# Performance work log

Measured on AMD Instinct MI355X. Metric: run time of the kernel, lower is better.

## Reference

```python
import jax, jax.numpy as jnp
import numpy as np

B, S, HID = 1, 2048, 2048
H, D = 16, 128
CACHE = 2048


def _rotate_half(x):
    x1, x2 = jnp.split(x, 2, axis=-1)
    return jnp.concatenate([-x2, x1], axis=-1)


def setup_inputs() -> dict:
    key = jax.random.key(0)
    ks = jax.random.split(key, 10)
    sc = 1.0 / np.sqrt(HID)
    return {
        "x": jax.random.normal(ks[0], (B, S, HID), jnp.float32),
        "wq": jax.random.normal(ks[1], (HID, H * D), jnp.float32) * sc,
        "wk": jax.random.normal(ks[2], (HID, H * D), jnp.float32) * sc,
        "wv": jax.random.normal(ks[3], (HID, H * D), jnp.float32) * sc,
        "wo": jax.random.normal(ks[4], (H * D, HID), jnp.float32) * sc,
        "cos": jax.random.uniform(ks[5], (1, 1, S, D), jnp.float32),
        "sin": jax.random.uniform(ks[6], (1, 1, S, D), jnp.float32),
        "attention_mask": jnp.zeros((B, 1, S, CACHE + S), jnp.float32),
        "k_cache": jax.random.normal(ks[7], (B, H, CACHE, D), jnp.float32),
        "v_cache": jax.random.normal(ks[8], (B, H, CACHE, D), jnp.float32),
    }


def reference(x, wq, wk, wv, wo, cos, sin, attention_mask, k_cache, v_cache):
    b, s, _ = x.shape
    # QKV projections -> [B, H, S, D]
    q = (x @ wq).reshape(b, s, H, D).transpose(0, 2, 1, 3)
    k = (x @ wk).reshape(b, s, H, D).transpose(0, 2, 1, 3)
    v = (x @ wv).reshape(b, s, H, D).transpose(0, 2, 1, 3)
    # inline RoPE (rotate-half)
    q = q * cos + _rotate_half(q) * sin
    k = k * cos + _rotate_half(k) * sin
    # KV-cache concat along sequence dim
    k = jnp.concatenate([k_cache, k], axis=2)
    v = jnp.concatenate([v_cache, v], axis=2)
    # manual scaled dot-product attention
    scale = 1.0 / np.sqrt(D).astype(np.float32)
    scores = jnp.einsum("bhqd,bhkd->bhqk", q, k) * scale + attention_mask
    attn = jax.nn.softmax(scores, axis=-1)
    ctx = jnp.einsum("bhqk,bhkd->bhqd", attn, v)  # [B,H,S,D]
    ctx = ctx.transpose(0, 2, 1, 3).reshape(b, s, H * D)
    return ctx @ wo
```

## Files before the change

### kernel.cpp

```cpp
#include <hip/hip_runtime.h>
#include <hip/hip_bf16.h>
#include <hip/hip_fp16.h>


typedef _Float16 half_t;
typedef __attribute__((ext_vector_type(8))) _Float16 f16x8;
typedef __attribute__((ext_vector_type(4))) _Float16 f16x4;
typedef __attribute__((ext_vector_type(4))) float f32x4;
typedef __attribute__((ext_vector_type(16))) float f32x16;

#define HIDN 2048
#define SEQ  2048
#define NH   16
#define HD   128
#define KVL  4096

#define VMCNT(n) asm volatile("s_waitcnt vmcnt(" #n ")" ::: "memory")

__device__ __forceinline__ void gll16(const void* g, void* l) {
  __builtin_amdgcn_global_load_lds(
      (const __attribute__((address_space(1))) void*)g,
      (__attribute__((address_space(3))) void*)l, 16, 0, 0);
}

__device__ __forceinline__ int pkrtz(float a, float b) {
  auto t = __builtin_amdgcn_cvt_pkrtz(a, b);
  return __builtin_bit_cast(int, t);
}

__global__ void k_prep(const float* __restrict__ x, half_t* __restrict__ x16,
                       const float* __restrict__ wq, const float* __restrict__ wk,
                       const float* __restrict__ wv, const float* __restrict__ wo,
                       half_t* __restrict__ wt_qkv, half_t* __restrict__ wt_o,
                       const float* __restrict__ kc, half_t* __restrict__ Kb,
                       const float* __restrict__ vc, half_t* __restrict__ Vt) {
  __shared__ float tile[64][65];
  int b = blockIdx.x;
  if (b < 2048) {
    int i = (b * 256 + threadIdx.x) * 8;
    float4 a = *reinterpret_cast<const float4*>(x + i);
    float4 c = *reinterpret_cast<const float4*>(x + i + 4);
    f16x8 o;
    o[0]=(half_t)a.x; o[1]=(half_t)a.y; o[2]=(half_t)a.z; o[3]=(half_t)a.w;
    o[4]=(half_t)c.x; o[5]=(half_t)c.y; o[6]=(half_t)c.z; o[7]=(half_t)c.w;
    *reinterpret_cast<f16x8*>(x16 + i) = o;
  } else if (b < 6144) {
    int idx = b - 2048;
    int z = idx >> 10, local = idx & 1023;
    int nx = local & 31, ky = local >> 5;
    const float* src = (z == 0) ? wq : (z == 1) ? wk : (z == 2) ? wv : wo;
    half_t* dst = (z < 3) ? (wt_qkv + (size_t)z * HIDN * HIDN) : wt_o;
    int n0 = nx * 64, k0 = ky * 64;
    int tx = threadIdx.x & 63, ty = threadIdx.x >> 6;
    #pragma unroll
    for (int j = 0; j < 64; j += 4) tile[ty + j][tx] = src[(k0 + ty + j) * HIDN + n0 + tx];
    __syncthreads();
    int ch = threadIdx.x & 7, nl = threadIdx.x >> 3;
    #pragma unroll
    for (int p = 0; p < 2; ++p) {
      int n_ = nl + p * 32;
      f16x8 v;
      #pragma unroll
      for (int e = 0; e < 8; ++e) v[e] = (half_t)tile[ch * 8 + e][n_];
      *reinterpret_cast<f16x8*>(&dst[(n0 + n_) * HIDN + k0 + ch * 8]) = v;
    }
  } else if (b < 8192) {
    int i = ((b - 6144) * 256 + threadIdx.x) * 8;
    int h = i >> 18, rem = i & 262143;
    float4 a = *reinterpret_cast<const float4*>(kc + i);
    float4 c = *reinterpret_cast<const float4*>(kc + i + 4);
    f16x8 o;
    o[0]=(half_t)a.x; o[1]=(half_t)a.y; o[2]=(half_t)a.z; o[3]=(half_t)a.w;
    o[4]=(half_t)c.x; o[5]=(half_t)c.y; o[6]=(half_t)c.z; o[7]=(half_t)c.w;
    *reinterpret_cast<f16x8*>(Kb + h * (KVL * HD) + rem) = o;
  } else {
    int idx = b - 8192;
    int kvx = idx & 31, dy = (idx >> 5) & 1, h = idx >> 6;
    int kv0 = kvx * 64, d0 = dy * 64;
    int tx = threadIdx.x & 63, ty = threadIdx.x >> 6;
    const float* src = vc + h * (2048 * HD);
    #pragma unroll
    for (int j = 0; j < 64; j += 4) tile[ty + j][tx] = src[(kv0 + ty + j) * HD + d0 + tx];
    __syncthreads();
    half_t* dst = Vt + h * (HD * KVL);
    int ch = threadIdx.x & 7, dl = threadIdx.x >> 3;
    #pragma unroll
    for (int p = 0; p < 2; ++p) {
      int d_ = dl + p * 32;
      f16x8 v;
      #pragma unroll
      for (int e = 0; e < 8; ++e) v[e] = (half_t)tile[ch * 8 + e][d_];
      *reinterpret_cast<f16x8*>(&dst[(d0 + d_) * KVL + kv0 + ch * 8]) = v;
    }
  }
}

__global__ void k_rope(half_t* __restrict__ Qb, half_t* __restrict__ Kb,
                       const float* __restrict__ cosb, const float* __restrict__ sinb) {
  int i = blockIdx.x * 256 + threadIdx.x;
  int s = i >> 10;
  int h = (i >> 6) & 15;
  int d = i & 63;
  float c1 = cosb[s * HD + d],      s1 = sinb[s * HD + d];
  float c2 = cosb[s * HD + d + 64], s2 = sinb[s * HD + d + 64];
  half_t* qp = Qb + s * HIDN + h * HD + d;
  float q1 = (float)qp[0], q2 = (float)qp[64];
  qp[0]  = (half_t)(q1 * c1 - q2 * s1);
  qp[64] = (half_t)(q2 * c2 + q1 * s2);
  half_t* kp = Kb + h * (KVL * HD) + (2048 + s) * HD + d;
  float k1 = (float)kp[0], k2 = (float)kp[64];
  kp[0]  = (half_t)(k1 * c1 - k2 * s1);
  kp[64] = (half_t)(k2 * c2 + k1 * s2);
}

__global__ __launch_bounds__(512, 1)
void k_gemm256(const half_t* __restrict__ A, const half_t* __restrict__ B,
               half_t* __restrict__ oQ, half_t* __restrict__ oK, half_t* __restrict__ oV) {
  __shared__ __align__(16) half_t sm[4][2][256 * 32];
  const int Kd = HIDN;
  int bx = blockIdx.x;
  int swz = (bx & 7) * 24 + (bx >> 3);
  int mt = swz / 24, nt = swz % 24;
  int m0 = mt * 256, n0 = nt * 256;
  int tid = threadIdx.x;
  int w = tid >> 6, l = tid & 63, lr = l & 15, lg = l >> 4;
  int waveM = (w >> 2) * 128, waveN = (w & 3) * 64;

  int r0 = tid >> 2, sl = tid & 3;
  const half_t* As0 = A + (m0 + r0) * Kd + ((sl ^ ((r0 >> 1) & 3)) * 8);
  const half_t* As1 = A + (m0 + r0 + 128) * Kd + ((sl ^ ((r0 >> 1) & 3)) * 8);
  const half_t* Bs0 = B + (n0 + r0) * Kd + ((sl ^ ((r0 >> 1) & 3)) * 8);
  const half_t* Bs1 = B + (n0 + r0 + 128) * Kd + ((sl ^ ((r0 >> 1) & 3)) * 8);

  f32x4 acc[8][4] = {};

  auto stage = [&](int buf, int kt) {
    int k0 = kt * 32;
    gll16(As0 + k0, (half_t*)sm[buf][0] + tid * 8);
    gll16(As1 + k0, (half_t*)sm[buf][0] + 4096 + tid * 8);
    gll16(Bs0 + k0, (half_t*)sm[buf][1] + tid * 8);
    gll16(Bs1 + k0, (half_t*)sm[buf][1] + 4096 + tid * 8);
  };
  auto compute = [&](int buf) {
    const half_t* Asm = sm[buf][0];
    const half_t* Bsm = sm[buf][1];
    f16x8 a[8], b2[4];
    #pragma unroll
    for (int f = 0; f < 8; ++f) {
      int rm = waveM + f * 16 + lr;
      a[f] = *reinterpret_cast<const f16x8*>(Asm + rm * 32 + ((lg ^ ((rm >> 1) & 3)) * 8));
    }
    #pragma unroll
    for (int f = 0; f < 4; ++f) {
      int rn = waveN + f * 16 + lr;
      b2[f] = *reinterpret_cast<const f16x8*>(Bsm + rn * 32 + ((lg ^ ((rn >> 1) & 3)) * 8));
    }
    #pragma unroll
    for (int fm = 0; fm < 8; ++fm)
      #pragma unroll
      for (int fn = 0; fn < 4; ++fn)
        acc[fm][fn] = __builtin_amdgcn_mfma_f32_16x16x32_f16(a[fm], b2[fn], acc[fm][fn], 0, 0, 0);
  };

  const int NKt = Kd / 32;
  stage(0, 0);
  stage(1, 1);
  for (int kt = 0; kt < NKt; ++kt) {
    if (kt + 2 < NKt) { stage((kt + 2) & 3, kt + 2); VMCNT(8); }
    else if (kt + 1 < NKt) VMCNT(4);
    else VMCNT(0);
    __builtin_amdgcn_s_barrier();
    compute(kt & 3);
  }

  #pragma unroll
  for (int fm = 0; fm < 8; ++fm) {
    int rbase = m0 + waveM + fm * 16 + lg * 4;
    #pragma unroll
    for (int fn = 0; fn < 4; ++fn) {
      int c = n0 + waveN + fn * 16 + lr;
      if (c < 2048) {
        #pragma unroll
        for (int i = 0; i < 4; ++i)
          oQ[(rbase + i) * HIDN + c] = (half_t)acc[fm][fn][i];
      } else if (c < 4096) {
        int c2 = c - 2048, hh = c2 >> 7, dd = c2 & 127;
        #pragma unroll
        for (int i = 0; i < 4; ++i)
          oK[hh * (KVL * HD) + (2048 + rbase + i) * HD + dd] = (half_t)acc[fm][fn][i];
      } else {
        int c2 = c - 4096, hh = c2 >> 7, dd = c2 & 127;
        f16x4 pk;
        #pragma unroll
        for (int i = 0; i < 4; ++i) pk[i] = (half_t)acc[fm][fn][i];
        *reinterpret_cast<f16x4*>(oV + hh * (HD * KVL) + dd * KVL + 2048 + rbase) = pk;
      }
    }
  }
}

template <int NT>
__global__ __launch_bounds__(256, 2)
void k_gemm_out(const half_t* __restrict__ A, const half_t* __restrict__ B,
                float* __restrict__ oF) {
  __shared__ __align__(16) half_t sm[4][2][128 * 32];
  const int Kd = HIDN;
  int nwg = gridDim.x, bx = blockIdx.x;
  int swz = (bx & 7) * (nwg >> 3) + (bx >> 3);
  int mt = swz / NT, nt = swz % NT;
  int m0 = mt * 128, n0 = nt * 128;
  int tid = threadIdx.x;
  int w = tid >> 6, l = tid & 63, lr = l & 15, lg = l >> 4;
  int waveM = (w >> 1) * 64, waveN = (w & 1) * 64;

  int r0 = tid >> 2, sl = tid & 3;
  int r1 = r0 + 64;
  const half_t* As0 = A + (m0 + r0) * Kd + ((sl ^ ((r0 >> 1) & 3)) * 8);
  const half_t* As1 = A + (m0 + r1) * Kd + ((sl ^ ((r1 >> 1) & 3)) * 8);
  const half_t* Bs0 = B + (n0 + r0) * Kd + ((sl ^ ((r0 >> 1) & 3)) * 8);
  const half_t* Bs1 = B + (n0 + r1) * Kd + ((sl ^ ((r1 >> 1) & 3)) * 8);

  f32x4 acc[4][4] = {};

  auto stage = [&](int buf, int kt) {
    int k0 = kt * 32;
    gll16(As0 + k0, (half_t*)sm[buf][0] + tid * 8);
    gll16(As1 + k0, (half_t*)sm[buf][0] + 2048 + tid * 8);
    gll16(Bs0 + k0, (half_t*)sm[buf][1] + tid * 8);
    gll16(Bs1 + k0, (half_t*)sm[buf][1] + 2048 + tid * 8);
  };
  auto compute = [&](int buf) {
    const half_t* Asm = sm[buf][0];
    const half_t* Bsm = sm[buf][1];
    f16x8 a[4], b[4];
    #pragma unroll
    for (int f = 0; f < 4; ++f) {
      int rm = waveM + f * 16 + lr;
      a[f] = *reinterpret_cast<const f16x8*>(Asm + rm * 32 + ((lg ^ ((rm >> 1) & 3)) * 8));
      int rn = waveN + f * 16 + lr;
      b[f] = *reinterpret_cast<const f16x8*>(Bsm + rn * 32 + ((lg ^ ((rn >> 1) & 3)) * 8));
    }
    #pragma unroll
    for (int fm = 0; fm < 4; ++fm)
      #pragma unroll
      for (int fn = 0; fn < 4; ++fn)
        acc[fm][fn] = __builtin_amdgcn_mfma_f32_16x16x32_f16(a[fm], b[fn], acc[fm][fn], 0, 0, 0);
  };

  const int NKt = Kd / 32;
  stage(0, 0);
  stage(1, 1);
  for (int kt = 0; kt < NKt; ++kt) {
    if (kt + 2 < NKt) { stage((kt + 2) & 3, kt + 2); VMCNT(8); }
    else if (kt + 1 < NKt) VMCNT(4);
    else VMCNT(0);
    __builtin_amdgcn_s_barrier();
    compute(kt & 3);
  }

  #pragma unroll
  for (int fm = 0; fm < 4; ++fm) {
    int rbase = m0 + waveM + fm * 16 + lg * 4;
    #pragma unroll
    for (int fn = 0; fn < 4; ++fn) {
      int c = n0 + waveN + fn * 16 + lr;
      #pragma unroll
      for (int i = 0; i < 4; ++i)
        oF[(rbase + i) * HIDN + c] = acc[fm][fn][i];
    }
  }
}

__global__ __launch_bounds__(512, 1)
void k_flash(const half_t* __restrict__ Qb, const half_t* __restrict__ Kb,
             const half_t* __restrict__ Vt,
             half_t* __restrict__ Po, float* __restrict__ Pl) {
  __shared__ __align__(16) half_t kt_s[8][32 * 128];
  __shared__ __align__(16) half_t vt_s[8][128 * 32];
  int b = blockIdx.x;
  int xcd = b & 7, kb = b >> 3;
  int h = xcd * 2 + (kb >> 4);
  int rem = kb & 15, qt = rem >> 1, half = rem & 1;
  int q0 = qt * 256;
  int tid = threadIdx.x, w = tid >> 6, l = tid & 63, lq = l & 31, hh = l >> 5;
  const half_t* Kh = Kb + h * (KVL * HD);
  const half_t* Vh = Vt + h * (HD * KVL);
  const int kvoff = half * 2048;

  int qrow = q0 + w * 32 + lq;
  f16x8 qf[8];
  #pragma unroll
  for (int ks = 0; ks < 8; ++ks) {
    qf[ks] = *reinterpret_cast<const f16x8*>(Qb + qrow * HIDN + h * HD + ks * 16 + hh * 8);
    #pragma unroll
    for (int e = 0; e < 8; ++e) qf[ks][e] *= (half_t)0.12751632f;
  }

  f32x16 Oa[4] = {};
  float l_i = 0.f;

  auto stage2 = [&](int s) {
    #pragma unroll
    for (int ti = 0; ti < 2; ++ti) {
      int t = s * 2 + ti, buf = t & 7;
      int kv0 = kvoff + t * 32;
      {
        int row = tid >> 4, c = tid & 15;
        gll16(Kh + (kv0 + row) * HD + ((c ^ (row & 15)) * 8), kt_s[buf] + tid * 8);
      }
      {
        int row = tid >> 2, c = tid & 3;
        gll16(Vh + row * KVL + kv0 + ((c ^ ((row >> 1) & 3)) * 8), vt_s[buf] + tid * 8);
      }
    }
  };

  auto tail1 = [&](f32x16& s0, const half_t* Vsm) {
    #pragma unroll
    for (int r = 0; r < 16; ++r) s0[r] = exp2f(s0[r]);
    float a8[8];
    #pragma unroll
    for (int r = 0; r < 8; ++r) a8[r] = s0[r] + s0[r + 8];
    #pragma unroll
    for (int st = 4; st > 0; st >>= 1)
      #pragma unroll
      for (int r = 0; r < 4; ++r)
        if (r < st) a8[r] += a8[r + st];
    l_i += a8[0];

    int pk_[8];
    #pragma unroll
    for (int r = 0; r < 8; ++r) pk_[r] = pkrtz(s0[2 * r], s0[2 * r + 1]);
    f16x8 pa[2];
    #pragma unroll
    for (int kk = 0; kk < 2; ++kk) {
      auto sA = __builtin_amdgcn_permlane32_swap(pk_[4 * kk + 0], pk_[4 * kk + 2], false, false);
      auto sB = __builtin_amdgcn_permlane32_swap(pk_[4 * kk + 1], pk_[4 * kk + 3], false, false);
      union { int i[4]; f16x8 v; } u;
      u.i[0] = sA[0]; u.i[1] = sB[0]; u.i[2] = sA[1]; u.i[3] = sB[1];
      pa[kk] = u.v;
    }

    __builtin_amdgcn_s_setprio(1);
    #pragma unroll
    for (int dt = 0; dt < 4; ++dt) {
      int row = dt * 32 + lq;
      #pragma unroll
      for (int kk = 0; kk < 2; ++kk) {
        f16x8 vb = *reinterpret_cast<const f16x8*>(
            Vsm + row * 32 + (((kk * 2 + hh) ^ ((row >> 1) & 3)) * 8));
        Oa[dt] = __builtin_amdgcn_mfma_f32_32x32x16_f16(pa[kk], vb, Oa[dt], 0, 0, 0);
      }
    }
    __builtin_amdgcn_s_setprio(0);
  };

  auto computePair = [&](int bufA, int bufB) {
    const half_t* KsA = kt_s[bufA];
    const half_t* KsB = kt_s[bufB];
    f32x16 sa, sb;
    #pragma unroll
    for (int i = 0; i < 16; ++i) { sa[i] = -8.0f; sb[i] = -8.0f; }
    __builtin_amdgcn_s_setprio(1);
    #pragma unroll
    for (int ks = 0; ks < 8; ++ks) {
      f16x8 a0 = *reinterpret_cast<const f16x8*>(
          KsA + lq * 128 + (((ks * 2 + hh) ^ (lq & 15)) * 8));
      sa = __builtin_amdgcn_mfma_f32_32x32x16_f16(a0, qf[ks], sa, 0, 0, 0);
    }
    #pragma unroll
    for (int ks = 0; ks < 8; ++ks) {
      f16x8 a0 = *reinterpret_cast<const f16x8*>(
          KsB + lq * 128 + (((ks * 2 + hh) ^ (lq & 15)) * 8));
      sb = __builtin_amdgcn_mfma_f32_32x32x16_f16(a0, qf[ks], sb, 0, 0, 0);
    }
    __builtin_amdgcn_s_setprio(0);
    tail1(sa, vt_s[bufA]);
    tail1(sb, vt_s[bufB]);
  };

  const int NSTEP = 32;
  stage2(0);
  stage2(1);
  for (int s = 0; s < NSTEP; ++s) {
    if (s + 2 < NSTEP) { stage2(s + 2); VMCNT(8); }
    else if (s + 1 < NSTEP) VMCNT(4);
    else VMCNT(0);
    __builtin_amdgcn_s_barrier();
    computePair((2 * s) & 7, (2 * s + 1) & 7);
  }

  size_t slot = (size_t)(half * 128 + h * 8 + qt);
  half_t* po = Po + slot * (256 * 128);
  float*  pl = Pl + slot * 512;
  pl[w * 64 + l] = l_i;
  #pragma unroll
  for (int j = 0; j < 16; ++j) {
    int qj = (j & 3) + 8 * (j >> 2) + 4 * hh;
    int q = w * 32 + qj;
    #pragma unroll
    for (int dt = 0; dt < 4; ++dt)
      po[q * 128 + dt * 32 + lq] = (half_t)Oa[dt][j];
  }
}

__global__ void k_fmerge(const half_t* __restrict__ Po, const float* __restrict__ Pl,
                         half_t* __restrict__ ctx) {
  int i = blockIdx.x * 256 + threadIdx.x;
  int col8 = i & 255;
  int s = i >> 8;
  int h = col8 >> 4, d0 = (col8 & 15) * 8;
  int qt = s >> 8, q = s & 255, qw = q >> 5, qj = q & 31;
  size_t slot0 = (size_t)(h * 8 + qt);
  size_t slot1 = slot0 + 128;
  f16x8 o0 = *reinterpret_cast<const f16x8*>(Po + slot0 * (256 * 128) + q * 128 + d0);
  f16x8 o1 = *reinterpret_cast<const f16x8*>(Po + slot1 * (256 * 128) + q * 128 + d0);
  float lsum = Pl[slot0 * 512 + qw * 64 + qj] + Pl[slot0 * 512 + qw * 64 + qj + 32] +
               Pl[slot1 * 512 + qw * 64 + qj] + Pl[slot1 * 512 + qw * 64 + qj + 32];
  float inv = 1.0f / lsum;
  f16x8 o;
  #pragma unroll
  for (int e = 0; e < 8; ++e)
    o[e] = (half_t)(((float)o0[e] + (float)o1[e]) * inv);
  *reinterpret_cast<f16x8*>(ctx + (size_t)s * HIDN + h * HD + d0) = o;
}


extern "C" void kernel_launch(void* const* d_in, const int* in_sizes, int n_in,
                              void* d_out, int out_size, void* d_ws, size_t ws_size,
                              hipStream_t stream) {
  const float* x    = (const float*)d_in[0];
  const float* wq   = (const float*)d_in[1];
  const float* wk   = (const float*)d_in[2];
  const float* wv   = (const float*)d_in[3];
  const float* wo   = (const float*)d_in[4];
  const float* cosb = (const float*)d_in[5];
  const float* sinb = (const float*)d_in[6];
  const float* kc   = (const float*)d_in[8];
  const float* vc   = (const float*)d_in[9];
  float* out = (float*)d_out;

  char* ws = (char*)d_ws;
  half_t* x16   = (half_t*)(ws);
  half_t* WtQKV = (half_t*)(ws + 8388608);
  half_t* Wto   = (half_t*)(ws + 33554432);
  half_t* Qb    = (half_t*)(ws + 41943040);
  half_t* Kb    = (half_t*)(ws + 50331648);
  half_t* Vtb   = (half_t*)(ws + 67108864);
  half_t* ctxb  = (half_t*)(ws + 83886080);
  half_t* Po    = (half_t*)(ws + 8388608);
  float*  Pl    = (float*)(ws + 8388608 + 16777216);

  k_prep<<<9216, 256, 0, stream>>>(x, x16, wq, wk, wv, wo, WtQKV, Wto, kc, Kb, vc, Vtb);
  k_gemm256<<<192, 512, 0, stream>>>(x16, WtQKV, Qb, Kb, Vtb);
  k_rope<<<8192, 256, 0, stream>>>(Qb, Kb, cosb, sinb);
  k_flash<<<256, 512, 0, stream>>>(Qb, Kb, Vtb, Po, Pl);
  k_fmerge<<<2048, 256, 0, stream>>>(Po, Pl, ctxb);
  k_gemm_out<16><<<16 * 16, 256, 0, stream>>>(ctxb, Wto, out);
}
```

Before: 204.5 us.

## Process two Q row tiles per wave and split KV into four chunks

Each wave in the flash kernel now holds two 32-row Q fragments and reuses every K/V tile loaded into shared memory for both, which halves LDS reads per MFMA. To keep 256 blocks, the KV range is split into four 1024-long chunks instead of two, and the first chunk writes its partial output straight into the context buffer. The merge kernel then sums four partials. The cost is more registers for the doubled accumulators and Q fragments, a four-stage LDS ring in place of eight, and more partial-output traffic through the merge.

```diff
diff --git a/kernel.cpp b/kernel.cpp
--- a/kernel.cpp
+++ b/kernel.cpp
@@ -274,48 +274,48 @@
 __global__ __launch_bounds__(512, 1)
 void k_flash(const half_t* __restrict__ Qb, const half_t* __restrict__ Kb,
              const half_t* __restrict__ Vt,
-             half_t* __restrict__ Po, float* __restrict__ Pl) {
-  __shared__ __align__(16) half_t kt_s[8][32 * 128];
-  __shared__ __align__(16) half_t vt_s[8][128 * 32];
+             half_t* __restrict__ Cp, half_t* __restrict__ Po, float* __restrict__ Pl) {
+  __shared__ __align__(16) half_t kt_s[4][32 * 128];
+  __shared__ __align__(16) half_t vt_s[4][128 * 32];
   int b = blockIdx.x;
   int xcd = b & 7, kb = b >> 3;
   int h = xcd * 2 + (kb >> 4);
-  int rem = kb & 15, qt = rem >> 1, half = rem & 1;
-  int q0 = qt * 256;
+  int rem = kb & 15, qt = rem >> 2, kvq = rem & 3;
+  int q0 = qt * 512;
   int tid = threadIdx.x, w = tid >> 6, l = tid & 63, lq = l & 31, hh = l >> 5;
   const half_t* Kh = Kb + h * (KVL * HD);
   const half_t* Vh = Vt + h * (HD * KVL);
-  const int kvoff = half * 2048;
-
-  int qrow = q0 + w * 32 + lq;
-  f16x8 qf[8];
+  const int kvoff = kvq * 1024;
+
+  int qrA = q0 + w * 64 + lq;
+  f16x8 qa[8], qb2[8];
   #pragma unroll
   for (int ks = 0; ks < 8; ++ks) {
-    qf[ks] = *reinterpret_cast<const f16x8*>(Qb + qrow * HIDN + h * HD + ks * 16 + hh * 8);
-    #pragma unroll
-    for (int e = 0; e < 8; ++e) qf[ks][e] *= (half_t)0.12751632f;
-  }
-
-  f32x16 Oa[4] = {};
-  float l_i = 0.f;
-
-  auto stage2 = [&](int s) {
-    #pragma unroll
-    for (int ti = 0; ti < 2; ++ti) {
-      int t = s * 2 + ti, buf = t & 7;
-      int kv0 = kvoff + t * 32;
-      {
-        int row = tid >> 4, c = tid & 15;
-        gll16(Kh + (kv0 + row) * HD + ((c ^ (row & 15)) * 8), kt_s[buf] + tid * 8);
-      }
-      {
-        int row = tid >> 2, c = tid & 3;
-        gll16(Vh + row * KVL + kv0 + ((c ^ ((row >> 1) & 3)) * 8), vt_s[buf] + tid * 8);
-      }
-    }
-  };
-
-  auto tail1 = [&](f32x16& s0, const half_t* Vsm) {
+    qa[ks]  = *reinterpret_cast<const f16x8*>(Qb + qrA * HIDN + h * HD + ks * 16 + hh * 8);
+    qb2[ks] = *reinterpret_cast<const f16x8*>(Qb + (qrA + 32) * HIDN + h * HD + ks * 16 + hh * 8);
+    #pragma unroll
+    for (int e = 0; e < 8; ++e) {
+      qa[ks][e]  *= (half_t)0.12751632f;
+      qb2[ks][e] *= (half_t)0.12751632f;
+    }
+  }
+
+  f32x16 OA[4] = {}, OB[4] = {};
+  float lA = 0.f, lB = 0.f;
+
+  auto stage1 = [&](int t) {
+    int buf = t & 3, kv0 = kvoff + t * 32;
+    {
+      int row = tid >> 4, c = tid & 15;
+      gll16(Kh + (kv0 + row) * HD + ((c ^ (row & 15)) * 8), kt_s[buf] + tid * 8);
+    }
+    {
+      int row = tid >> 2, c = tid & 3;
+      gll16(Vh + row * KVL + kv0 + ((c ^ ((row >> 1) & 3)) * 8), vt_s[buf] + tid * 8);
+    }
+  };
+
+  auto tailSM = [&](f32x16& s0, float& l_i, f16x8* pa) {
     #pragma unroll
     for (int r = 0; r < 16; ++r) s0[r] = exp2f(s0[r]);
     float a8[8];
@@ -327,11 +327,9 @@
       for (int r = 0; r < 4; ++r)
         if (r < st) a8[r] += a8[r + st];
     l_i += a8[0];
-
     int pk_[8];
     #pragma unroll
     for (int r = 0; r < 8; ++r) pk_[r] = pkrtz(s0[2 * r], s0[2 * r + 1]);
-    f16x8 pa[2];
     #pragma unroll
     for (int kk = 0; kk < 2; ++kk) {
       auto sA = __builtin_amdgcn_permlane32_swap(pk_[4 * kk + 0], pk_[4 * kk + 2], false, false);
@@ -340,7 +338,26 @@
       u.i[0] = sA[0]; u.i[1] = sB[0]; u.i[2] = sA[1]; u.i[3] = sB[1];
       pa[kk] = u.v;
     }
-
+  };
+
+  auto computeT = [&](int buf) {
+    const half_t* Ksm = kt_s[buf];
+    const half_t* Vsm = vt_s[buf];
+    f32x16 sa, sb;
+    #pragma unroll
+    for (int i = 0; i < 16; ++i) { sa[i] = -8.0f; sb[i] = -8.0f; }
+    __builtin_amdgcn_s_setprio(1);
+    #pragma unroll
+    for (int ks = 0; ks < 8; ++ks) {
+      f16x8 a0 = *reinterpret_cast<const f16x8*>(
+          Ksm + lq * 128 + (((ks * 2 + hh) ^ (lq & 15)) * 8));
+      sa = __builtin_amdgcn_mfma_f32_32x32x16_f16(a0, qa[ks], sa, 0, 0, 0);
+      sb = __builtin_amdgcn_mfma_f32_32x32x16_f16(a0, qb2[ks], sb, 0, 0, 0);
+    }
+    __builtin_amdgcn_s_setprio(0);
+    f16x8 paA[2], paB[2];
+    tailSM(sa, lA, paA);
+    tailSM(sb, lB, paB);
     __builtin_amdgcn_s_setprio(1);
     #pragma unroll
     for (int dt = 0; dt < 4; ++dt) {
@@ -349,79 +366,80 @@
       for (int kk = 0; kk < 2; ++kk) {
         f16x8 vb = *reinterpret_cast<const f16x8*>(
             Vsm + row * 32 + (((kk * 2 + hh) ^ ((row >> 1) & 3)) * 8));
-        Oa[dt] = __builtin_amdgcn_mfma_f32_32x32x16_f16(pa[kk], vb, Oa[dt], 0, 0, 0);
+        OA[dt] = __builtin_amdgcn_mfma_f32_32x32x16_f16(paA[kk], vb, OA[dt], 0, 0, 0);
+        OB[dt] = __builtin_amdgcn_mfma_f32_32x32x16_f16(paB[kk], vb, OB[dt], 0, 0, 0);
       }
     }
     __builtin_amdgcn_s_setprio(0);
   };
 
-  auto computePair = [&](int bufA, int bufB) {
-    const half_t* KsA = kt_s[bufA];
-    const half_t* KsB = kt_s[bufB];
-    f32x16 sa, sb;
-    #pragma unroll
-    for (int i = 0; i < 16; ++i) { sa[i] = -8.0f; sb[i] = -8.0f; }
-    __builtin_amdgcn_s_setprio(1);
-    #pragma unroll
-    for (int ks = 0; ks < 8; ++ks) {
-      f16x8 a0 = *reinterpret_cast<const f16x8*>(
-          KsA + lq * 128 + (((ks * 2 + hh) ^ (lq & 15)) * 8));
-      sa = __builtin_amdgcn_mfma_f32_32x32x16_f16(a0, qf[ks], sa, 0, 0, 0);
-    }
-    #pragma unroll
-    for (int ks = 0; ks < 8; ++ks) {
-      f16x8 a0 = *reinterpret_cast<const f16x8*>(
-          KsB + lq * 128 + (((ks * 2 + hh) ^ (lq & 15)) * 8));
-      sb = __builtin_amdgcn_mfma_f32_32x32x16_f16(a0, qf[ks], sb, 0, 0, 0);
-    }
-    __builtin_amdgcn_s_setprio(0);
-    tail1(sa, vt_s[bufA]);
-    tail1(sb, vt_s[bufB]);
-  };
-
-  const int NSTEP = 32;
-  stage2(0);
-  stage2(1);
-  for (int s = 0; s < NSTEP; ++s) {
-    if (s + 2 < NSTEP) { stage2(s + 2); VMCNT(8); }
-    else if (s + 1 < NSTEP) VMCNT(4);
+  const int NT = 32;
+  stage1(0);
+  stage1(1);
+  for (int t = 0; t < NT; ++t) {
+    if (t + 2 < NT) { stage1(t + 2); VMCNT(2); }
+    else if (t + 1 < NT) VMCNT(2);
     else VMCNT(0);
     __builtin_amdgcn_s_barrier();
-    computePair((2 * s) & 7, (2 * s + 1) & 7);
-  }
-
-  size_t slot = (size_t)(half * 128 + h * 8 + qt);
-  half_t* po = Po + slot * (256 * 128);
-  float*  pl = Pl + slot * 512;
-  pl[w * 64 + l] = l_i;
-  #pragma unroll
-  for (int j = 0; j < 16; ++j) {
-    int qj = (j & 3) + 8 * (j >> 2) + 4 * hh;
-    int q = w * 32 + qj;
-    #pragma unroll
-    for (int dt = 0; dt < 4; ++dt)
-      po[q * 128 + dt * 32 + lq] = (half_t)Oa[dt][j];
-  }
-}
-
-__global__ void k_fmerge(const half_t* __restrict__ Po, const float* __restrict__ Pl,
-                         half_t* __restrict__ ctx) {
+    computeT(t & 3);
+  }
+
+  float* pl = Pl + (size_t)(kvq * 64 + h * 4 + qt) * 1024;
+  pl[hh * 512 + w * 64 + lq] = lA;
+  pl[hh * 512 + w * 64 + 32 + lq] = lB;
+  if (kvq == 0) {
+    #pragma unroll
+    for (int j = 0; j < 16; ++j) {
+      int qj = (j & 3) + 8 * (j >> 2) + 4 * hh;
+      int qA = q0 + w * 64 + qj;
+      #pragma unroll
+      for (int dt = 0; dt < 4; ++dt) {
+        Cp[(size_t)qA * HIDN + h * HD + dt * 32 + lq] = (half_t)OA[dt][j];
+        Cp[(size_t)(qA + 32) * HIDN + h * HD + dt * 32 + lq] = (half_t)OB[dt][j];
+      }
+    }
+  } else {
+    half_t* po = Po + (size_t)((kvq - 1) * 64 + h * 4 + qt) * 65536;
+    #pragma unroll
+    for (int j = 0; j < 16; ++j) {
+      int qj = (j & 3) + 8 * (j >> 2) + 4 * hh;
+      int qA = w * 64 + qj;
+      #pragma unroll
+      for (int dt = 0; dt < 4; ++dt) {
+        po[qA * 128 + dt * 32 + lq] = (half_t)OA[dt][j];
+        po[(qA + 32) * 128 + dt * 32 + lq] = (half_t)OB[dt][j];
+      }
+    }
+  }
+}
+
+__global__ void k_fmerge(half_t* __restrict__ ctx, const half_t* __restrict__ Po,
+                         const float* __restrict__ Pl) {
   int i = blockIdx.x * 256 + threadIdx.x;
-  int col8 = i & 255;
-  int s = i >> 8;
+  int col8 = i & 255, s = i >> 8;
   int h = col8 >> 4, d0 = (col8 & 15) * 8;
-  int qt = s >> 8, q = s & 255, qw = q >> 5, qj = q & 31;
-  size_t slot0 = (size_t)(h * 8 + qt);
-  size_t slot1 = slot0 + 128;
-  f16x8 o0 = *reinterpret_cast<const f16x8*>(Po + slot0 * (256 * 128) + q * 128 + d0);
-  f16x8 o1 = *reinterpret_cast<const f16x8*>(Po + slot1 * (256 * 128) + q * 128 + d0);
-  float lsum = Pl[slot0 * 512 + qw * 64 + qj] + Pl[slot0 * 512 + qw * 64 + qj + 32] +
-               Pl[slot1 * 512 + qw * 64 + qj] + Pl[slot1 * 512 + qw * 64 + qj + 32];
+  int qt = s >> 9, lcq = s & 511;
+  f16x8 o0 = *reinterpret_cast<const f16x8*>(ctx + (size_t)s * HIDN + h * HD + d0);
+  float acc[8];
+  #pragma unroll
+  for (int e = 0; e < 8; ++e) acc[e] = (float)o0[e];
+  #pragma unroll
+  for (int k = 1; k < 4; ++k) {
+    const half_t* po = Po + (size_t)((k - 1) * 64 + h * 4 + qt) * 65536;
+    f16x8 ok = *reinterpret_cast<const f16x8*>(po + lcq * 128 + d0);
+    #pragma unroll
+    for (int e = 0; e < 8; ++e) acc[e] += (float)ok[e];
+  }
+  float lsum = 0.f;
+  #pragma unroll
+  for (int k = 0; k < 4; ++k) {
+    const float* pl = Pl + (size_t)(k * 64 + h * 4 + qt) * 1024;
+    lsum += pl[lcq] + pl[512 + lcq];
+  }
   float inv = 1.0f / lsum;
   f16x8 o;
   #pragma unroll
-  for (int e = 0; e < 8; ++e)
-    o[e] = (half_t)(((float)o0[e] + (float)o1[e]) * inv);
+  for (int e = 0; e < 8; ++e) o[e] = (half_t)(acc[e] * inv);
   *reinterpret_cast<f16x8*>(ctx + (size_t)s * HIDN + h * HD + d0) = o;
 }
 
@@ -448,13 +466,13 @@
   half_t* Kb    = (half_t*)(ws + 50331648);
   half_t* Vtb   = (half_t*)(ws + 67108864);
   half_t* ctxb  = (half_t*)(ws + 83886080);
-  half_t* Po    = (half_t*)(ws + 8388608);
-  float*  Pl    = (float*)(ws + 8388608 + 16777216);
+  half_t* Po    = (half_t*)(ws);
+  float*  Pl    = (float*)(ws + 25165824);
 
   k_prep<<<9216, 256, 0, stream>>>(x, x16, wq, wk, wv, wo, WtQKV, Wto, kc, Kb, vc, Vtb);
   k_gemm256<<<192, 512, 0, stream>>>(x16, WtQKV, Qb, Kb, Vtb);
   k_rope<<<8192, 256, 0, stream>>>(Qb, Kb, cosb, sinb);
-  k_flash<<<256, 512, 0, stream>>>(Qb, Kb, Vtb, Po, Pl);
-  k_fmerge<<<2048, 256, 0, stream>>>(Po, Pl, ctxb);
+  k_flash<<<256, 512, 0, stream>>>(Qb, Kb, Vtb, ctxb, Po, Pl);
+  k_fmerge<<<2048, 256, 0, stream>>>(ctxb, Po, Pl);
   k_gemm_out<16><<<16 * 16, 256, 0, stream>>>(ctxb, Wto, out);
 }
```

New measurement: 249.5 us. 1.22x slower.
